# Optimization experiments

Measured on AMD Instinct MI355X. Metric: run time of the kernel, lower is better.

Reference implementation:

```python
import jax, jax.numpy as jnp
import numpy as np

B, L = 2, 1024
N_EMBD = 768
D_FF = 4 * N_EMBD
N_EXPERT = 8
TOPK = 2
N_PREDICT = 2
LB_COEF = 0.01
KL_COEF = 1.0


def setup_inputs() -> dict:
    key = jax.random.key(0)
    k0, k1, k2, k3, k4 = jax.random.split(key, 5)
    s = 0.02
    x = jax.random.normal(k0, (B, L, N_EMBD), dtype=jnp.float32)
    Wg_prior = jax.random.normal(k1, (N_EMBD, N_EXPERT), dtype=jnp.float32) * s
    Wg_post = jax.random.normal(k2, (N_EMBD, N_EXPERT), dtype=jnp.float32) * s
    W_fc = jax.random.normal(k3, (N_EXPERT, N_EMBD, D_FF), dtype=jnp.float32) * s
    W_proj = jax.random.normal(k4, (N_EXPERT, D_FF, N_EMBD), dtype=jnp.float32) * s
    return {"x": x, "Wg_prior": Wg_prior, "Wg_post": Wg_post, "W_fc": W_fc, "W_proj": W_proj}


def reference(x, Wg_prior, Wg_post, W_fc, W_proj):
    b, l, h = x.shape
    x_flat = x.reshape(-1, h)                              # [N, h], N = b*l
    prior_logits = x_flat @ Wg_prior                       # [N, E]

    # lookforward: shift by N_PREDICT, pad tail with last token (training path, l > n)
    n = N_PREDICT
    x_future = jnp.concatenate(
        [x[:, n:, :], jnp.broadcast_to(x[:, -1:, :], (b, n, h))], axis=1)
    posterior_logits = x_future.reshape(-1, h) @ Wg_post   # [N, E]
    router_logits = posterior_logits                       # train: route with posterior

    expert_weights = jax.nn.softmax(router_logits, axis=-1)          # [N, E]
    selected_weights, selected_experts = jax.lax.top_k(expert_weights, TOPK)
    selected_weights = selected_weights / selected_weights.sum(-1, keepdims=True)

    onehot = jax.nn.one_hot(selected_experts, N_EXPERT, dtype=x.dtype)  # [N, K, E]
    combine = (onehot * selected_weights[..., None]).sum(axis=1)        # [N, E]

    # dispatch/combine: loop over the small fixed expert set (structurally distinct weights)
    out = jnp.zeros_like(x_flat)
    for e in range(N_EXPERT):
        h1 = jnp.square(jax.nn.relu(x_flat @ W_fc[e]))     # [N, 4h] relu(x)^2
        out = out + combine[:, e:e + 1] * (h1 @ W_proj[e])
    x_new = out.reshape(b, l, h)

    # load-balance aux loss
    num_tokens = b * l
    counts = onehot.sum(axis=(0, 1))                       # tokens assigned per expert
    f = counts / (num_tokens * TOPK)
    P = expert_weights.mean(axis=0)
    lb_loss = N_EXPERT * (f * P).sum() * LB_COEF

    # KL(posterior || prior)
    prior_lp = jax.nn.log_softmax(prior_logits, axis=-1)
    post_lp = jax.nn.log_softmax(posterior_logits, axis=-1)
    kl = (jnp.exp(post_lp) * (post_lp - prior_lp)).sum(-1).mean() * KL_COEF

    aux_loss = lb_loss + kl
    return x_new, aux_loss
```

## Files before the change

kernel.cpp:

```cpp
#include <hip/hip_runtime.h>
#include <hip/hip_bf16.h>

typedef __attribute__((ext_vector_type(8))) short short8v;
typedef __attribute__((ext_vector_type(4))) float f32x4;
typedef __attribute__((ext_vector_type(4))) int int4v;

#define NTOK  2048
#define NEMBD 768
#define DFF   3072
#define NEXP  8
#define MAXSLOT 5120
#define NT1 24
#define NT2 6
#define MAXT1 40
#define MAXT2 80
#define NTRB  2304

#define WS_XBF   0
#define WS_GATES (WS_XBF + (size_t)NTOK*NEMBD*2)
#define WS_TE    (WS_GATES + NTOK*8*4)
#define WS_TW    (WS_TE + NTOK*2*4)
#define WS_KL    (WS_TW + NTOK*2*4)
#define WS_CTRL  (WS_KL + NTOK*4)
#define WS_STOK  (WS_CTRL + 2048)
#define WS_TSLOT (WS_STOK + MAXSLOT*4)
#define WS_WFCT  (WS_TSLOT + NTOK*2*4)
#define WS_WPT   (WS_WFCT + (size_t)NEXP*DFF*NEMBD*2)
#define WS_H     (WS_WPT + (size_t)NEXP*NEMBD*DFF*2)
#define WS_OBUF  WS_WFCT

__device__ __forceinline__ unsigned short f2bf(float f) {
    union { float f; unsigned u; } v; v.f = f;
    unsigned r = v.u + 0x7fffu + ((v.u >> 16) & 1u);
    return (unsigned short)(r >> 16);
}

__device__ __forceinline__ void gload16(const void* g, void* l) {
    __builtin_amdgcn_global_load_lds(
        (const __attribute__((address_space(1))) void*)g,
        (__attribute__((address_space(3))) void*)l, 16, 0, 0);
}

__global__ __launch_bounds__(256) void k_front(
    const float* __restrict__ x, const float* __restrict__ WgP, const float* __restrict__ WgQ,
    const float* __restrict__ Wfc, const float* __restrict__ Wpj,
    unsigned short* __restrict__ WfcT, unsigned short* __restrict__ WpT,
    unsigned short* __restrict__ xbf, float* __restrict__ gates,
    int* __restrict__ te, float* __restrict__ tw, float* __restrict__ kl_tok)
{
    __shared__ unsigned short sT[64 * 32 * 8];
    int tid = threadIdx.x;
    int bid = blockIdx.x;
    if (bid < NTRB) {
        const float* in; unsigned short* out; int R, C, tilesC;
        if (bid < NTRB / 2) { in = Wfc; out = WfcT; R = NEMBD; C = DFF; tilesC = 48; }
        else { bid -= NTRB / 2; in = Wpj; out = WpT; R = DFF; C = NEMBD; tilesC = 12; }
        int e = bid / 144, rem = bid % 144;
        int rt = rem / tilesC, ct = rem % tilesC;
        int ng = tid & 7, kg = tid >> 3;
        const float* src = in + ((size_t)e * R + rt * 256 + kg * 8) * C + ct * 64 + ng * 8;
        unsigned short cb[8][8];
        #pragma unroll
        for (int i = 0; i < 8; ++i) {
            float4 a = *(const float4*)&src[(size_t)i * C];
            float4 b = *(const float4*)&src[(size_t)i * C + 4];
            cb[0][i] = f2bf(a.x); cb[1][i] = f2bf(a.y); cb[2][i] = f2bf(a.z); cb[3][i] = f2bf(a.w);
            cb[4][i] = f2bf(b.x); cb[5][i] = f2bf(b.y); cb[6][i] = f2bf(b.z); cb[7][i] = f2bf(b.w);
        }
        #pragma unroll
        for (int j = 0; j < 8; ++j) {
            int n = ng * 8 + j;
            int sl = kg ^ j;
            *(int4v*)&sT[((size_t)n * 32 + sl) * 8] = *(const int4v*)&cb[j][0];
        }
        __syncthreads();
        unsigned short* dstp = out + ((size_t)e * C + ct * 64) * R + rt * 256;
        int n2 = tid >> 2, cs = tid & 3;
        #pragma unroll
        for (int i = 0; i < 8; ++i) {
            int s = cs * 8 + i;
            int sl = s ^ (n2 & 7);
            *(int4v*)&dstp[(size_t)n2 * R + s * 8] = *(const int4v*)&sT[((size_t)n2 * 32 + sl) * 8];
        }
        return;
    }
    int rb = bid - NTRB;
    int wave = tid >> 6, lane = tid & 63;
    int t = rb * 4 + wave;
    int b = t >> 10, l = t & 1023;
    int lf = l + 2; if (lf > 1023) lf = 1023;
    const float* xr = x + (size_t)t * NEMBD;
    const float* xf = x + (size_t)((b << 10) + lf) * NEMBD;
    int e = lane & 7, kg = lane >> 3;

    float accP = 0.f, accQ = 0.f;
    #pragma unroll 8
    for (int i = 0; i < 96; ++i) {
        int k = kg + 8 * i;
        accP += xr[k] * WgP[k * NEXP + e];
        accQ += xf[k] * WgQ[k * NEXP + e];
    }
    #pragma unroll
    for (int off = 8; off < 64; off <<= 1) {
        accP += __shfl_xor(accP, off);
        accQ += __shfl_xor(accQ, off);
    }
    float mq = accQ, mp = accP;
    #pragma unroll
    for (int off = 1; off < 8; off <<= 1) {
        mq = fmaxf(mq, __shfl_xor(mq, off));
        mp = fmaxf(mp, __shfl_xor(mp, off));
    }
    float gq = __expf(accQ - mq), gp = __expf(accP - mp);
    float se = gq, sp = gp;
    #pragma unroll
    for (int off = 1; off < 8; off <<= 1) {
        se += __shfl_xor(se, off);
        sp += __shfl_xor(sp, off);
    }
    float v0 = gq; int e0 = e;
    #pragma unroll
    for (int off = 1; off < 8; off <<= 1) {
        float ov = __shfl_xor(v0, off); int oe = __shfl_xor(e0, off);
        if (ov > v0 || (ov == v0 && oe < e0)) { v0 = ov; e0 = oe; }
    }
    float vx = (e == e0) ? -1.f : gq;
    float v1 = vx; int e1 = e;
    #pragma unroll
    for (int off = 1; off < 8; off <<= 1) {
        float ov = __shfl_xor(v1, off); int oe = __shfl_xor(e1, off);
        if (ov > v1 || (ov == v1 && oe < e1)) { v1 = ov; e1 = oe; }
    }
    float lq = (accQ - mq) - logf(se);
    float lp = (accP - mp) - logf(sp);
    float kl = __expf(lq) * (lq - lp);
    #pragma unroll
    for (int off = 1; off < 8; off <<= 1) kl += __shfl_xor(kl, off);

    if (lane < 8) gates[t * NEXP + e] = gq / se;
    if (lane == 0) {
        float s2 = v0 + v1;
        te[t * 2] = e0; te[t * 2 + 1] = e1;
        tw[t * 2] = v0 / s2; tw[t * 2 + 1] = v1 / s2;
        kl_tok[t] = kl;
    }
    const float4* xs4 = (const float4*)(x + (size_t)rb * 4 * NEMBD);
    ushort4* xd4 = (ushort4*)(xbf + (size_t)rb * 4 * NEMBD);
    for (int i = tid; i < 4 * NEMBD / 4; i += 256) {
        float4 v = xs4[i];
        ushort4 o;
        o.x = f2bf(v.x); o.y = f2bf(v.y); o.z = f2bf(v.z); o.w = f2bf(v.w);
        xd4[i] = o;
    }
}

__global__ __launch_bounds__(256) void k_sched(
    const int* __restrict__ te, int* __restrict__ ctrl,
    int* __restrict__ stok, int* __restrict__ tslot)
{
    __shared__ int cur[NEXP];
    __shared__ int cnt_s[NEXP];
    __shared__ int sOff[NEXP];
    int tid = threadIdx.x, lane = tid & 63;
    if (tid < NEXP) { cur[tid] = 0; cnt_s[tid] = 0; }
    for (int i = tid; i < MAXSLOT; i += 256) stok[i] = 0;
    __syncthreads();
    int cc[NEXP];
    #pragma unroll
    for (int e = 0; e < NEXP; ++e) cc[e] = 0;
    for (int i = tid; i < NTOK * 2; i += 256) {
        int e = te[i];
        #pragma unroll
        for (int q = 0; q < NEXP; ++q) cc[q] += (e == q) ? 1 : 0;
    }
    #pragma unroll
    for (int e = 0; e < NEXP; ++e) {
        int v = cc[e];
        #pragma unroll
        for (int off = 32; off; off >>= 1) v += __shfl_xor(v, off);
        if (lane == 0) atomicAdd(&cnt_s[e], v);
    }
    __syncthreads();
    if (tid == 0) {
        int off = 0, n1 = 0, n2 = 0;
        for (int e = 0; e < NEXP; ++e) {
            int cnt = cnt_s[e];
            ctrl[e] = cnt;
            ctrl[16 + e] = off; sOff[e] = off;
            int t128 = (cnt + 127) >> 7;
            for (int m = 0; m < t128; ++m)     ctrl[64 + n1++]  = (e << 16) | m;
            for (int m = 0; m < 2 * t128; ++m) ctrl[128 + n2++] = (e << 16) | m;
            off += t128 << 7;
        }
        ctrl[24] = off; ctrl[25] = n1; ctrl[26] = n2;
    }
    __syncthreads();
    for (int t = tid; t < NTOK; t += 256) {
        #pragma unroll
        for (int k = 0; k < 2; ++k) {
            int e = te[t * 2 + k];
            int s = atomicAdd(&cur[e], 1);
            int flat = sOff[e] + s;
            stok[flat] = t; tslot[t * 2 + k] = flat;
        }
    }
}

__global__ __launch_bounds__(256) void k_gemm1(
    const unsigned short* __restrict__ xbf, const unsigned short* __restrict__ WfcT,
    const int* __restrict__ ctrl, const int* __restrict__ slot_tok,
    unsigned short* __restrict__ H)
{
    int bx = blockIdx.x;
    int swz = (bx & 7) * (MAXT1 * NT1 / 8) + (bx >> 3);
    int nt = swz / MAXT1, tI = swz % MAXT1;
    if (tI >= ctrl[25]) return;
    int pk = ctrl[64 + tI];
    int e = pk >> 16, mt = pk & 0xffff;
    int base = ctrl[16 + e] + (mt << 7);

    __shared__ unsigned short sAB[2 * 128 * 64];
    unsigned short* sA = sAB;
    unsigned short* sB = sAB + 128 * 64;

    int tid = threadIdx.x, w = tid >> 6, lane = tid & 63;
    int wr = w >> 1, wc = w & 1;

    int swsub = (((lane & 7) ^ ((lane >> 3) & 7)) << 3);
    const unsigned short* wfc = WfcT + ((size_t)e * DFF + nt * 128) * NEMBD;
    const unsigned short* aptr[4]; const unsigned short* bptr[4];
    #pragma unroll
    for (int i = 0; i < 4; ++i) {
        int r = i * 32 + w * 8 + (lane >> 3);
        aptr[i] = xbf + (size_t)slot_tok[base + r] * NEMBD + swsub;
        bptr[i] = wfc + (size_t)r * NEMBD + swsub;
    }

    f32x4 acc[4][4];
    #pragma unroll
    for (int i = 0; i < 4; ++i)
        #pragma unroll
        for (int j = 0; j < 4; ++j) acc[i][j] = (f32x4){0.f, 0.f, 0.f, 0.f};

    int rsw = (lane & 7) << 3;
    for (int kk = 0; kk < NEMBD; kk += 64) {
        #pragma unroll
        for (int i = 0; i < 4; ++i) {
            gload16(aptr[i] + kk, &sA[(i * 256 + w * 64) * 8]);
            gload16(bptr[i] + kk, &sB[(i * 256 + w * 64) * 8]);
        }
        __syncthreads();
        #pragma unroll
        for (int kh = 0; kh < 2; ++kh) {
            int c = (kh * 32 + ((lane >> 4) << 3)) ^ rsw;
            short8v af[4], bfv[4];
            #pragma unroll
            for (int m = 0; m < 4; ++m)
                af[m] = *(const short8v*)&sA[(wr * 64 + m * 16 + (lane & 15)) * 64 + c];
            #pragma unroll
            for (int n = 0; n < 4; ++n)
                bfv[n] = *(const short8v*)&sB[(wc * 64 + n * 16 + (lane & 15)) * 64 + c];
            #pragma unroll
            for (int m = 0; m < 4; ++m)
                #pragma unroll
                for (int n = 0; n < 4; ++n)
                    acc[m][n] = __builtin_amdgcn_mfma_f32_16x16x32_bf16(af[m], bfv[n], acc[m][n], 0, 0, 0);
        }
        __syncthreads();
    }

    unsigned short* sC = sAB;
    #pragma unroll
    for (int m = 0; m < 4; ++m)
        #pragma unroll
        for (int n = 0; n < 4; ++n) {
            int col = wc * 64 + n * 16 + (lane & 15);
            #pragma unroll
            for (int i = 0; i < 4; ++i) {
                int row = wr * 64 + m * 16 + (lane >> 4) * 4 + i;
                float v = acc[m][n][i];
                v = v > 0.f ? v * v : 0.f;
                sC[row * 128 + col] = f2bf(v);
            }
        }
    __syncthreads();
    #pragma unroll
    for (int it = 0; it < 8; ++it) {
        int idx = tid + it * 256;
        int row = idx >> 4, j = idx & 15;
        *(int4v*)&H[(size_t)(base + row) * DFF + nt * 128 + j * 8] =
            *(const int4v*)&sC[row * 128 + j * 8];
    }
}

__global__ __launch_bounds__(256) void k_gemm2(
    const unsigned short* __restrict__ H, const unsigned short* __restrict__ WpT,
    const int* __restrict__ ctrl, float* __restrict__ obuf)
{
    int bx = blockIdx.x;
    int swz = (bx & 7) * (MAXT2 * NT2 / 8) + (bx >> 3);
    int nt = swz / MAXT2, tI = swz % MAXT2;
    if (tI >= ctrl[26]) return;
    int pk = ctrl[128 + tI];
    int e = pk >> 16, mt = pk & 0xffff;
    int base = ctrl[16 + e] + (mt << 6);

    __shared__ unsigned short sA[64 * 64];
    __shared__ unsigned short sB[128 * 64];

    int tid = threadIdx.x, w = tid >> 6, lane = tid & 63;
    int wr = w >> 1, wc = w & 1;

    int swsub = (((lane & 7) ^ ((lane >> 3) & 7)) << 3);
    const unsigned short* wp = WpT + ((size_t)e * NEMBD + nt * 128) * DFF;
    const unsigned short* aptr[2]; const unsigned short* bptr[4];
    #pragma unroll
    for (int i = 0; i < 2; ++i) {
        int r = i * 32 + w * 8 + (lane >> 3);
        aptr[i] = H + (size_t)(base + r) * DFF + swsub;
    }
    #pragma unroll
    for (int i = 0; i < 4; ++i) {
        int r = i * 32 + w * 8 + (lane >> 3);
        bptr[i] = wp + (size_t)r * DFF + swsub;
    }

    f32x4 acc[2][4];
    #pragma unroll
    for (int i = 0; i < 2; ++i)
        #pragma unroll
        for (int j = 0; j < 4; ++j) acc[i][j] = (f32x4){0.f, 0.f, 0.f, 0.f};

    int rsw = (lane & 7) << 3;
    for (int kk = 0; kk < DFF; kk += 64) {
        #pragma unroll
        for (int i = 0; i < 2; ++i)
            gload16(aptr[i] + kk, &sA[(i * 256 + w * 64) * 8]);
        #pragma unroll
        for (int i = 0; i < 4; ++i)
            gload16(bptr[i] + kk, &sB[(i * 256 + w * 64) * 8]);
        __syncthreads();
        #pragma unroll
        for (int kh = 0; kh < 2; ++kh) {
            int c = (kh * 32 + ((lane >> 4) << 3)) ^ rsw;
            short8v af[2], bfv[4];
            #pragma unroll
            for (int m = 0; m < 2; ++m)
                af[m] = *(const short8v*)&sA[(wr * 32 + m * 16 + (lane & 15)) * 64 + c];
            #pragma unroll
            for (int n = 0; n < 4; ++n)
                bfv[n] = *(const short8v*)&sB[(wc * 64 + n * 16 + (lane & 15)) * 64 + c];
            #pragma unroll
            for (int m = 0; m < 2; ++m)
                #pragma unroll
                for (int n = 0; n < 4; ++n)
                    acc[m][n] = __builtin_amdgcn_mfma_f32_16x16x32_bf16(af[m], bfv[n], acc[m][n], 0, 0, 0);
        }
        __syncthreads();
    }

    #pragma unroll
    for (int m = 0; m < 2; ++m)
        #pragma unroll
        for (int n = 0; n < 4; ++n) {
            int col = nt * 128 + wc * 64 + n * 16 + (lane & 15);
            #pragma unroll
            for (int i = 0; i < 4; ++i) {
                int row = wr * 32 + m * 16 + (lane >> 4) * 4 + i;
                obuf[(size_t)(base + row) * NEMBD + col] = acc[m][n][i];
            }
        }
}

__global__ __launch_bounds__(256) void k_finish(
    const float* __restrict__ obuf, const int* __restrict__ tslot,
    const float* __restrict__ tw, const float* __restrict__ gates,
    const float* __restrict__ kl_tok, const int* __restrict__ ctrl,
    float* __restrict__ out)
{
    int tid = threadIdx.x;
    if (blockIdx.x == 512) {
        __shared__ float sred[256];
        float p[NEXP]; float kls = 0.f;
        #pragma unroll
        for (int e = 0; e < NEXP; ++e) p[e] = 0.f;
        for (int t = tid; t < NTOK; t += 256) {
            #pragma unroll
            for (int e = 0; e < NEXP; ++e) p[e] += gates[t * NEXP + e];
            kls += kl_tok[t];
        }
        float Ps[NEXP];
        for (int e = 0; e < NEXP; ++e) {
            sred[tid] = p[e]; __syncthreads();
            for (int s = 128; s; s >>= 1) { if (tid < s) sred[tid] += sred[tid + s]; __syncthreads(); }
            if (tid == 0) Ps[e] = sred[0];
            __syncthreads();
        }
        sred[tid] = kls; __syncthreads();
        for (int s = 128; s; s >>= 1) { if (tid < s) sred[tid] += sred[tid + s]; __syncthreads(); }
        if (tid == 0) {
            float kl_mean = sred[0] / (float)NTOK;
            float lb = 0.f;
            for (int e = 0; e < NEXP; ++e)
                lb += ((float)ctrl[e] / (float)(NTOK * 2)) * (Ps[e] / (float)NTOK);
            lb *= (float)NEXP * 0.01f;
            out[(size_t)NTOK * NEMBD] = lb + kl_mean;
        }
        return;
    }
    int wave = tid >> 6, lane = tid & 63;
    int t = blockIdx.x * 4 + wave;
    int s0 = tslot[t * 2], s1 = tslot[t * 2 + 1];
    float g0 = tw[t * 2], g1 = tw[t * 2 + 1];
    const float4* r0 = (const float4*)(obuf + (size_t)s0 * NEMBD);
    const float4* r1 = (const float4*)(obuf + (size_t)s1 * NEMBD);
    float4* o4 = (float4*)(out + (size_t)t * NEMBD);
    #pragma unroll
    for (int j = 0; j < 3; ++j) {
        int c = j * 64 + lane;
        float4 a = r0[c], b = r1[c];
        float4 o;
        o.x = g0 * a.x + g1 * b.x; o.y = g0 * a.y + g1 * b.y;
        o.z = g0 * a.z + g1 * b.z; o.w = g0 * a.w + g1 * b.w;
        o4[c] = o;
    }
}

extern "C" void kernel_launch(void* const* d_in, const int* in_sizes, int n_in,
                              void* d_out, int out_size, void* d_ws, size_t ws_size,
                              hipStream_t stream) {
    const float* x   = (const float*)d_in[0];
    const float* WgP = (const float*)d_in[1];
    const float* WgQ = (const float*)d_in[2];
    const float* Wfc = (const float*)d_in[3];
    const float* Wpj = (const float*)d_in[4];
    float* out = (float*)d_out;

    char* ws = (char*)d_ws;
    unsigned short* xbf  = (unsigned short*)(ws + WS_XBF);
    float* gates = (float*)(ws + WS_GATES);
    int*   te    = (int*)(ws + WS_TE);
    float* tw    = (float*)(ws + WS_TW);
    float* klt   = (float*)(ws + WS_KL);
    int*   ctrl  = (int*)(ws + WS_CTRL);
    int*   stok  = (int*)(ws + WS_STOK);
    int*   tslot = (int*)(ws + WS_TSLOT);
    unsigned short* WfcT = (unsigned short*)(ws + WS_WFCT);
    unsigned short* WpT  = (unsigned short*)(ws + WS_WPT);
    unsigned short* H    = (unsigned short*)(ws + WS_H);
    float* obuf  = (float*)(ws + WS_OBUF);

    k_front<<<NTRB + 512, 256, 0, stream>>>(
        x, WgP, WgQ, Wfc, Wpj, WfcT, WpT, xbf, gates, te, tw, klt);
    k_sched<<<1, 256, 0, stream>>>(te, ctrl, stok, tslot);
    k_gemm1<<<MAXT1 * NT1, 256, 0, stream>>>(xbf, WfcT, ctrl, stok, H);
    k_gemm2<<<MAXT2 * NT2, 256, 0, stream>>>(H, WpT, ctrl, obuf);
    k_finish<<<513, 256, 0, stream>>>(obuf, tslot, tw, gates, klt, ctrl, out);
}
```

Measured before the change: 160.1 us.

## Move W_proj transpose into gemm1 launch to overlap with expert GEMM

Splits the front kernel so it only transposes W_fc alongside routing, and appends the W_proj fp32-to-bf16 transpose blocks to the first expert GEMM launch. The memory-bound transpose can then overlap with compute-bound GEMM work instead of running before the scheduler. The risk is that the transpose blocks sit after the GEMM blocks in the grid and may run mostly in the tail, and that they share the GEMM's LDS allocation.

Measured after the change: 158.6 us. Within noise of the previous version (-1.0%).

```diff
diff --git a/kernel.cpp b/kernel.cpp
--- a/kernel.cpp
+++ b/kernel.cpp
@@ -14,7 +14,6 @@
 #define NT2 6
 #define MAXT1 40
 #define MAXT2 80
-#define NTRB  2304
 
 #define WS_XBF   0
 #define WS_GATES (WS_XBF + (size_t)NTOK*NEMBD*2)
@@ -41,50 +40,53 @@
         (__attribute__((address_space(3))) void*)l, 16, 0, 0);
 }
 
-__global__ __launch_bounds__(256) void k_front(
+__device__ __forceinline__ void transpose_tile(
+    const float* __restrict__ in, unsigned short* __restrict__ out,
+    int R, int C, int tilesC, int tb, unsigned short* sT, int tid)
+{
+    int e = tb / 144, rem = tb % 144;
+    int rt = rem / tilesC, ct = rem % tilesC;
+    int ng = tid & 7, kg = tid >> 3;
+    const float* src = in + ((size_t)e * R + rt * 256 + kg * 8) * C + ct * 64 + ng * 8;
+    unsigned short cb[8][8];
+    #pragma unroll
+    for (int i = 0; i < 8; ++i) {
+        float4 a = *(const float4*)&src[(size_t)i * C];
+        float4 b = *(const float4*)&src[(size_t)i * C + 4];
+        cb[0][i] = f2bf(a.x); cb[1][i] = f2bf(a.y); cb[2][i] = f2bf(a.z); cb[3][i] = f2bf(a.w);
+        cb[4][i] = f2bf(b.x); cb[5][i] = f2bf(b.y); cb[6][i] = f2bf(b.z); cb[7][i] = f2bf(b.w);
+    }
+    #pragma unroll
+    for (int j = 0; j < 8; ++j) {
+        int n = ng * 8 + j;
+        int sl = kg ^ j;
+        *(int4v*)&sT[((size_t)n * 32 + sl) * 8] = *(const int4v*)&cb[j][0];
+    }
+    __syncthreads();
+    unsigned short* dstp = out + ((size_t)e * C + ct * 64) * R + rt * 256;
+    int n2 = tid >> 2, cs = tid & 3;
+    #pragma unroll
+    for (int i = 0; i < 8; ++i) {
+        int s = cs * 8 + i;
+        int sl = s ^ (n2 & 7);
+        *(int4v*)&dstp[(size_t)n2 * R + s * 8] = *(const int4v*)&sT[((size_t)n2 * 32 + sl) * 8];
+    }
+}
+
+__global__ __launch_bounds__(256) void k_frontA(
     const float* __restrict__ x, const float* __restrict__ WgP, const float* __restrict__ WgQ,
-    const float* __restrict__ Wfc, const float* __restrict__ Wpj,
-    unsigned short* __restrict__ WfcT, unsigned short* __restrict__ WpT,
+    const float* __restrict__ Wfc, unsigned short* __restrict__ WfcT,
     unsigned short* __restrict__ xbf, float* __restrict__ gates,
     int* __restrict__ te, float* __restrict__ tw, float* __restrict__ kl_tok)
 {
     __shared__ unsigned short sT[64 * 32 * 8];
     int tid = threadIdx.x;
     int bid = blockIdx.x;
-    if (bid < NTRB) {
-        const float* in; unsigned short* out; int R, C, tilesC;
-        if (bid < NTRB / 2) { in = Wfc; out = WfcT; R = NEMBD; C = DFF; tilesC = 48; }
-        else { bid -= NTRB / 2; in = Wpj; out = WpT; R = DFF; C = NEMBD; tilesC = 12; }
-        int e = bid / 144, rem = bid % 144;
-        int rt = rem / tilesC, ct = rem % tilesC;
-        int ng = tid & 7, kg = tid >> 3;
-        const float* src = in + ((size_t)e * R + rt * 256 + kg * 8) * C + ct * 64 + ng * 8;
-        unsigned short cb[8][8];
-        #pragma unroll
-        for (int i = 0; i < 8; ++i) {
-            float4 a = *(const float4*)&src[(size_t)i * C];
-            float4 b = *(const float4*)&src[(size_t)i * C + 4];
-            cb[0][i] = f2bf(a.x); cb[1][i] = f2bf(a.y); cb[2][i] = f2bf(a.z); cb[3][i] = f2bf(a.w);
-            cb[4][i] = f2bf(b.x); cb[5][i] = f2bf(b.y); cb[6][i] = f2bf(b.z); cb[7][i] = f2bf(b.w);
-        }
-        #pragma unroll
-        for (int j = 0; j < 8; ++j) {
-            int n = ng * 8 + j;
-            int sl = kg ^ j;
-            *(int4v*)&sT[((size_t)n * 32 + sl) * 8] = *(const int4v*)&cb[j][0];
-        }
-        __syncthreads();
-        unsigned short* dstp = out + ((size_t)e * C + ct * 64) * R + rt * 256;
-        int n2 = tid >> 2, cs = tid & 3;
-        #pragma unroll
-        for (int i = 0; i < 8; ++i) {
-            int s = cs * 8 + i;
-            int sl = s ^ (n2 & 7);
-            *(int4v*)&dstp[(size_t)n2 * R + s * 8] = *(const int4v*)&sT[((size_t)n2 * 32 + sl) * 8];
-        }
+    if (bid >= 512) {
+        transpose_tile(Wfc, WfcT, NEMBD, DFF, 48, bid - 512, sT, tid);
         return;
     }
-    int rb = bid - NTRB;
+    int rb = bid;
     int wave = tid >> 6, lane = tid & 63;
     int t = rb * 4 + wave;
     int b = t >> 10, l = t & 1023;
@@ -206,12 +208,20 @@
     }
 }
 
-__global__ __launch_bounds__(256) void k_gemm1(
+__global__ __launch_bounds__(256) void k_midB(
     const unsigned short* __restrict__ xbf, const unsigned short* __restrict__ WfcT,
+    const float* __restrict__ Wpj, unsigned short* __restrict__ WpT,
     const int* __restrict__ ctrl, const int* __restrict__ slot_tok,
     unsigned short* __restrict__ H)
 {
-    int bx = blockIdx.x;
+    __shared__ unsigned short sAB[2 * 128 * 64];
+    int tid = threadIdx.x;
+    int bid = blockIdx.x;
+    if (bid >= 960) {
+        transpose_tile(Wpj, WpT, DFF, NEMBD, 12, bid - 960, sAB, tid);
+        return;
+    }
+    int bx = bid;
     int swz = (bx & 7) * (MAXT1 * NT1 / 8) + (bx >> 3);
     int nt = swz / MAXT1, tI = swz % MAXT1;
     if (tI >= ctrl[25]) return;
@@ -219,11 +229,10 @@
     int e = pk >> 16, mt = pk & 0xffff;
     int base = ctrl[16 + e] + (mt << 7);
 
-    __shared__ unsigned short sAB[2 * 128 * 64];
     unsigned short* sA = sAB;
     unsigned short* sB = sAB + 128 * 64;
 
-    int tid = threadIdx.x, w = tid >> 6, lane = tid & 63;
+    int w = tid >> 6, lane = tid & 63;
     int wr = w >> 1, wc = w & 1;
 
     int swsub = (((lane & 7) ^ ((lane >> 3) & 7)) << 3);
@@ -450,10 +459,10 @@
     unsigned short* H    = (unsigned short*)(ws + WS_H);
     float* obuf  = (float*)(ws + WS_OBUF);
 
-    k_front<<<NTRB + 512, 256, 0, stream>>>(
-        x, WgP, WgQ, Wfc, Wpj, WfcT, WpT, xbf, gates, te, tw, klt);
+    k_frontA<<<512 + 1152, 256, 0, stream>>>(
+        x, WgP, WgQ, Wfc, WfcT, xbf, gates, te, tw, klt);
     k_sched<<<1, 256, 0, stream>>>(te, ctrl, stok, tslot);
-    k_gemm1<<<MAXT1 * NT1, 256, 0, stream>>>(xbf, WfcT, ctrl, stok, H);
+    k_midB<<<960 + 1152, 256, 0, stream>>>(xbf, WfcT, Wpj, WpT, ctrl, stok, H);
     k_gemm2<<<MAXT2 * NT2, 256, 0, stream>>>(H, WpT, ctrl, obuf);
     k_finish<<<513, 256, 0, stream>>>(obuf, tslot, tw, gates, klt, ctrl, out);
 }
```
